# Performance work log

Measured on AMD Instinct MI355X. Metric: run time of the kernel, lower is better.

## Reference

```python
import jax, jax.numpy as jnp
import numpy as np

B, D_IN, D_H, N = 16, 32, 64, 4000
ORDER = 2
C_CAT = D_IN + D_H            # 96 channels into each gate conv
C_EFF = (ORDER + 1) * C_CAT   # 288 after order-K diffusion concat


def setup_inputs() -> dict:
    key = jax.random.key(0)
    ks = jax.random.split(key, 9)
    x = jax.random.normal(ks[0], (B, D_IN, N), dtype=jnp.float32)
    h = jax.random.normal(ks[1], (B, D_H, N), dtype=jnp.float32)
    # uniform adjacency, roughly row-normalized to keep diffusion stable
    adj = jax.random.uniform(ks[2], (N, N), dtype=jnp.float32) / N
    scale = 0.05
    Wf = jax.random.normal(ks[3], (D_H, C_EFF), dtype=jnp.float32) * scale
    Wu = jax.random.normal(ks[4], (D_H, C_EFF), dtype=jnp.float32) * scale
    Wc = jax.random.normal(ks[5], (D_H, C_EFF), dtype=jnp.float32) * scale
    bf = jax.random.normal(ks[6], (D_H,), dtype=jnp.float32) * scale
    bu = jax.random.normal(ks[7], (D_H,), dtype=jnp.float32) * scale
    bc = jax.random.normal(ks[8], (D_H,), dtype=jnp.float32) * scale
    return {"x": x, "h": h, "adj": adj, "Wf": Wf, "bf": bf,
            "Wu": Wu, "bu": bu, "Wc": Wc, "bc": bc}


def _spatial_conv(z, adj, W, b):
    # z: [b, c, n]; order-2 diffusion: concat [z, A z, A^2 z] then 1x1 conv
    z1 = jnp.einsum('mn,bcn->bcm', adj, z)
    z2 = jnp.einsum('mn,bcn->bcm', adj, z1)
    feats = jnp.concatenate([z, z1, z2], axis=1)           # [b, 3c, n]
    return jnp.einsum('oc,bcn->bon', W, feats) + b[None, :, None]


def reference(x, h, adj, Wf, bf, Wu, bu, Wc, bc):
    x_gates = jnp.concatenate([x, h], axis=1)              # [b, d_in+d_h, n]
    r = jax.nn.sigmoid(_spatial_conv(x_gates, adj, Wf, bf))
    u = jax.nn.sigmoid(_spatial_conv(x_gates, adj, Wu, bu))
    x_c = jnp.concatenate([x, r * h], axis=1)
    c = jnp.tanh(_spatial_conv(x_c, adj, Wc, bc))
    return u * h + (1.0 - u) * c
```

## Files before the change

kernel.cpp:

```cpp
#include <hip/hip_runtime.h>
#include <cstdint>


#define NREAL 4000
#define NPAD  4096

typedef unsigned short u16;
typedef __attribute__((ext_vector_type(8))) short short8;
typedef __attribute__((ext_vector_type(4))) float f32x4;
typedef __attribute__((ext_vector_type(4))) unsigned short u16x4;

__device__ __forceinline__ u16 f2bf(float f) {
  unsigned u = __builtin_bit_cast(unsigned, f);
  return (u16)((u + 0x7FFFu + ((u >> 16) & 1u)) >> 16);
}
__device__ __forceinline__ float bf2f(u16 b) {
  unsigned u = ((unsigned)b) << 16;
  return __builtin_bit_cast(float, u);
}

__global__ __launch_bounds__(256) void k_pack_adj(const float* __restrict__ adj,
                                                  u16* __restrict__ out) {
  const int idx = blockIdx.x * 256 + threadIdx.x;
  const int m = idx >> 10;
  const int n0 = (idx & 1023) << 2;
  u16x4 o;
  if (m < NREAL && n0 < NREAL) {
    const float4 v = *reinterpret_cast<const float4*>(&adj[(long)m * NREAL + n0]);
    o.x = f2bf(v.x); o.y = f2bf(v.y); o.z = f2bf(v.z); o.w = f2bf(v.w);
  } else {
    o.x = 0; o.y = 0; o.z = 0; o.w = 0;
  }
  *reinterpret_cast<u16x4*>(&out[(long)m * NPAD + n0]) = o;
}

__global__ __launch_bounds__(256) void k_pack_zg(const float* __restrict__ x,
                                                 const float* __restrict__ h,
                                                 u16* __restrict__ zg) {
  const int idx = blockIdx.x * 256 + threadIdx.x;
  const int row = idx >> 10;
  const int n0 = (idx & 1023) << 2;
  const int b = row / 96, c = row % 96;
  const float* src = (c < 32) ? &x[((long)b * 32 + c) * NREAL]
                              : &h[((long)b * 64 + (c - 32)) * NREAL];
  u16x4 o;
  if (n0 < NREAL) {
    const float4 v = *reinterpret_cast<const float4*>(&src[n0]);
    o.x = f2bf(v.x); o.y = f2bf(v.y); o.z = f2bf(v.z); o.w = f2bf(v.w);
  } else {
    o.x = 0; o.y = 0; o.z = 0; o.w = 0;
  }
  *reinterpret_cast<u16x4*>(&zg[(long)row * NPAD + n0]) = o;
}

__global__ __launch_bounds__(256) void k_pack_w(const float* __restrict__ Wf,
                                                const float* __restrict__ Wu,
                                                const float* __restrict__ Wc,
                                                float* __restrict__ Wgt,
                                                float* __restrict__ Wct) {
  const int idx = blockIdx.x * 256 + threadIdx.x;
  if (idx < 288 * 128) {
    const int c = idx >> 7, o = idx & 127;
    Wgt[idx] = (o < 64) ? Wf[o * 288 + c] : Wu[(o - 64) * 288 + c];
  }
  if (idx < 288 * 64) {
    const int c = idx >> 6, o = idx & 63;
    Wct[idx] = Wc[o * 288 + c];
  }
}

#define GLDS(dst, src)                                                         \
  __builtin_amdgcn_global_load_lds(                                            \
      (const __attribute__((address_space(1))) void*)(src),                    \
      (__attribute__((address_space(3))) void*)(dst), 16, 0, 0)

template<bool F32OUT>
__global__ __launch_bounds__(512, 2) void k_gemm256(const u16* __restrict__ A,
                                                    const u16* __restrict__ B,
                                                    void* __restrict__ Cout,
                                                    int ktPerChunk, long chunkElems) {
  __shared__ __align__(16) u16 As[2][256 * 64];
  __shared__ __align__(16) u16 Bs[2][256 * 64];
  const int tid = threadIdx.x;
  const int lane = tid & 63;
  const int wv = tid >> 6;
  const int wm = wv >> 2;
  const int wn = wv & 3;

  const int srow = tid >> 3;
  const int jlog = (tid & 7) ^ (srow & 7);
  const long kt0 = (long)blockIdx.z * ktPerChunk * 64;
  const u16* aB = A + (long)(blockIdx.y * 256 + srow) * NPAD + kt0 + jlog * 8;
  const u16* bB = B + (long)(blockIdx.x * 256 + srow) * NPAD + kt0 + jlog * 8;
  const int ldst = tid * 8;

  const int fr = lane & 15;
  const int swz = (fr & 7) << 4;
  const int kb0 = (((lane >> 4) << 4)) ^ swz;
  const int kb1 = (64 + ((lane >> 4) << 4)) ^ swz;

  f32x4 acc[8][4] = {};
  const int T = ktPerChunk;

  GLDS(&Bs[0][0 + ldst],     bB);
  GLDS(&Bs[0][4096 + ldst],  bB + 64L * NPAD);
  GLDS(&Bs[0][8192 + ldst],  bB + 128L * NPAD);
  GLDS(&Bs[0][12288 + ldst], bB + 192L * NPAD);
  GLDS(&As[0][0 + ldst],     aB);
  GLDS(&As[0][8192 + ldst],  aB + 128L * NPAD);
  GLDS(&As[0][4096 + ldst],  aB + 64L * NPAD);
  GLDS(&As[0][12288 + ldst], aB + 192L * NPAD);
  asm volatile("s_waitcnt vmcnt(0)" ::: "memory");
  __builtin_amdgcn_s_barrier();
  __builtin_amdgcn_sched_barrier(0);

  for (int t = 0; t < T; ++t) {
    const int bsel = t & 1;
    const char* Ab = (const char*)&As[bsel][0];
    const char* Bb = (const char*)&Bs[bsel][0];
    u16* An = &As[bsel ^ 1][0];
    u16* Bn = &Bs[bsel ^ 1][0];
    const bool more = (t + 1 < T);
    const long ko = (long)(t + 1) * 64;
    short8 bv[4][2];
#pragma unroll
    for (int p = 0; p < 4; ++p) {
      if (more) {
        if (p == 0) { GLDS(Bn + ldst, bB + ko);
                      GLDS(Bn + 4096 + ldst, bB + 64L * NPAD + ko); }
        if (p == 1) { GLDS(Bn + 8192 + ldst, bB + 128L * NPAD + ko);
                      GLDS(Bn + 12288 + ldst, bB + 192L * NPAD + ko); }
        if (p == 2) { GLDS(An + ldst, aB + ko);
                      GLDS(An + 8192 + ldst, aB + 128L * NPAD + ko); }
        if (p == 3) { GLDS(An + 4096 + ldst, aB + 64L * NPAD + ko);
                      GLDS(An + 12288 + ldst, aB + 192L * NPAD + ko); }
      }
      asm volatile("" ::: "memory");
      if (p == 0) {
#pragma unroll
        for (int ni = 0; ni < 4; ++ni) {
          const int brow = (wn << 6) + (ni << 4) + fr;
          bv[ni][0] = *(const short8*)(Bb + brow * 128 + kb0);
          bv[ni][1] = *(const short8*)(Bb + brow * 128 + kb1);
        }
      }
      short8 av[2][2];
#pragma unroll
      for (int q = 0; q < 2; ++q) {
        const int arow = (wm << 7) + ((2 * p + q) << 4) + fr;
        av[q][0] = *(const short8*)(Ab + arow * 128 + kb0);
        av[q][1] = *(const short8*)(Ab + arow * 128 + kb1);
      }
      __builtin_amdgcn_s_setprio(1);
#pragma unroll
      for (int q = 0; q < 2; ++q)
#pragma unroll
        for (int ni = 0; ni < 4; ++ni) {
          acc[2 * p + q][ni] = __builtin_amdgcn_mfma_f32_16x16x32_bf16(
              av[q][0], bv[ni][0], acc[2 * p + q][ni], 0, 0, 0);
          acc[2 * p + q][ni] = __builtin_amdgcn_mfma_f32_16x16x32_bf16(
              av[q][1], bv[ni][1], acc[2 * p + q][ni], 0, 0, 0);
        }
      __builtin_amdgcn_s_setprio(0);
      if (p == 1) {
        if (more) asm volatile("s_waitcnt vmcnt(4)" ::: "memory");
        else      asm volatile("s_waitcnt vmcnt(0)" ::: "memory");
        __builtin_amdgcn_s_barrier();
        __builtin_amdgcn_sched_barrier(0);
      }
      if (p == 3 && more) {
        asm volatile("s_waitcnt vmcnt(2)" ::: "memory");
        __builtin_amdgcn_s_barrier();
        __builtin_amdgcn_sched_barrier(0);
      }
    }
  }

  const int rb = blockIdx.y * 256 + (wm << 7) + ((lane >> 4) << 2);
  const int cb = blockIdx.x * 256 + (wn << 6) + fr;
  if (F32OUT) {
    float* C = (float*)Cout + (long)blockIdx.z * chunkElems;
#pragma unroll
    for (int mi = 0; mi < 8; ++mi)
#pragma unroll
      for (int ni = 0; ni < 4; ++ni)
#pragma unroll
        for (int q = 0; q < 4; ++q)
          C[(long)(rb + (mi << 4) + q) * NPAD + cb + (ni << 4)] = acc[mi][ni][q];
  } else {
    u16* C = (u16*)Cout;
#pragma unroll
    for (int mi = 0; mi < 8; ++mi)
#pragma unroll
      for (int ni = 0; ni < 4; ++ni)
#pragma unroll
        for (int q = 0; q < 4; ++q)
          C[(long)(rb + (mi << 4) + q) * NPAD + cb + (ni << 4)] = f2bf(acc[mi][ni][q]);
  }
}

template<int NC>
__global__ __launch_bounds__(256) void k_combine(const float* __restrict__ P,
                                                 long chunkElems,
                                                 u16* __restrict__ out) {
  const long i4 = ((long)blockIdx.x * 256 + threadIdx.x) * 4;
  f32x4 s = *reinterpret_cast<const f32x4*>(&P[i4]);
#pragma unroll
  for (int c = 1; c < NC; ++c) {
    const f32x4 v = *reinterpret_cast<const f32x4*>(&P[(long)c * chunkElems + i4]);
    s.x += v.x; s.y += v.y; s.z += v.z; s.w += v.w;
  }
  u16x4 o;
  o.x = f2bf(s.x); o.y = f2bf(s.y); o.z = f2bf(s.z); o.w = f2bf(s.w);
  *reinterpret_cast<u16x4*>(&out[i4]) = o;
}

__global__ __launch_bounds__(512) void k_gates(
    const float* __restrict__ x, const float* __restrict__ h,
    const float* __restrict__ Wgt,
    const float* __restrict__ bfv, const float* __restrict__ buv,
    const u16* __restrict__ Z1, const u16* __restrict__ Z2,
    u16* __restrict__ rh_bf, float* __restrict__ rh_f, float* __restrict__ u_f) {
  const int lane = threadIdx.x & 63;
  const int wq = __builtin_amdgcn_readfirstlane(threadIdx.x >> 6);
  const int b = blockIdx.y;
  const int n0 = blockIdx.x * 128 + (lane << 1);
  if (n0 >= NREAL) return;
  const int ob = wq << 4;
  const float* xb = x + (long)b * 32 * NREAL + n0;
  const float* hb = h + (long)b * 64 * NREAL + n0;
  const u16* z1b = Z1 + (long)b * 96 * NPAD + n0;
  const u16* z2b = Z2 + (long)b * 96 * NPAD + n0;

  float a0[16] = {}, a1[16] = {};
#pragma unroll 4
  for (int c = 0; c < 32; ++c) {
    const float2 f = *reinterpret_cast<const float2*>(&xb[(long)c * NREAL]);
#pragma unroll
    for (int oi = 0; oi < 16; ++oi) {
      const float w = Wgt[c * 128 + ob + oi];
      a0[oi] = fmaf(w, f.x, a0[oi]); a1[oi] = fmaf(w, f.y, a1[oi]);
    }
  }
#pragma unroll 4
  for (int c = 0; c < 64; ++c) {
    const float2 f = *reinterpret_cast<const float2*>(&hb[(long)c * NREAL]);
#pragma unroll
    for (int oi = 0; oi < 16; ++oi) {
      const float w = Wgt[(32 + c) * 128 + ob + oi];
      a0[oi] = fmaf(w, f.x, a0[oi]); a1[oi] = fmaf(w, f.y, a1[oi]);
    }
  }
#pragma unroll 4
  for (int c = 0; c < 96; ++c) {
    const unsigned pv = *reinterpret_cast<const unsigned*>(&z1b[(long)c * NPAD]);
    const float f0 = bf2f((u16)(pv & 0xffff)), f1 = bf2f((u16)(pv >> 16));
#pragma unroll
    for (int oi = 0; oi < 16; ++oi) {
      const float w = Wgt[(96 + c) * 128 + ob + oi];
      a0[oi] = fmaf(w, f0, a0[oi]); a1[oi] = fmaf(w, f1, a1[oi]);
    }
  }
#pragma unroll 4
  for (int c = 0; c < 96; ++c) {
    const unsigned pv = *reinterpret_cast<const unsigned*>(&z2b[(long)c * NPAD]);
    const float f0 = bf2f((u16)(pv & 0xffff)), f1 = bf2f((u16)(pv >> 16));
#pragma unroll
    for (int oi = 0; oi < 16; ++oi) {
      const float w = Wgt[(192 + c) * 128 + ob + oi];
      a0[oi] = fmaf(w, f0, a0[oi]); a1[oi] = fmaf(w, f1, a1[oi]);
    }
  }

  if (wq < 4) {
#pragma unroll
    for (int oi = 0; oi < 16; ++oi) {
      const int og = ob + oi;
      const float bb = bfv[og];
      const float r0 = 1.f / (1.f + __expf(-(a0[oi] + bb)));
      const float r1 = 1.f / (1.f + __expf(-(a1[oi] + bb)));
      const float2 hv = *reinterpret_cast<const float2*>(&hb[(long)og * NREAL]);
      const float rh0 = r0 * hv.x, rh1 = r1 * hv.y;
      if (rh_f)
        *reinterpret_cast<float2*>(&rh_f[((long)b * 64 + og) * NREAL + n0]) =
            make_float2(rh0, rh1);
      const unsigned pk = (unsigned)f2bf(rh0) | ((unsigned)f2bf(rh1) << 16);
      *reinterpret_cast<unsigned*>(&rh_bf[((long)b * 64 + og) * NPAD + n0]) = pk;
    }
  } else {
#pragma unroll
    for (int oi = 0; oi < 16; ++oi) {
      const int og = (ob - 64) + oi;
      const float bb = buv[og];
      const float u0 = 1.f / (1.f + __expf(-(a0[oi] + bb)));
      const float u1 = 1.f / (1.f + __expf(-(a1[oi] + bb)));
      *reinterpret_cast<float2*>(&u_f[((long)b * 64 + og) * NREAL + n0]) =
          make_float2(u0, u1);
    }
  }
}

template<bool RHF32>
__global__ __launch_bounds__(512) void k_cand(
    const float* __restrict__ x, const float* __restrict__ h,
    const float* __restrict__ Wct, const float* __restrict__ bcv,
    const u16* __restrict__ Z1, const u16* __restrict__ Z2,
    const u16* __restrict__ Rhb, const u16* __restrict__ Rh1,
    const u16* __restrict__ Rh2,
    const float* __restrict__ rh_f, const float* __restrict__ u_f,
    float* __restrict__ out) {
  const int lane = threadIdx.x & 63;
  const int wq = __builtin_amdgcn_readfirstlane(threadIdx.x >> 6);
  const int ob = (wq & 3) << 4;
  const int n = blockIdx.x * 128 + ((wq >> 2) << 6) + lane;
  const int b = blockIdx.y;
  if (n >= NREAL) return;
  const float* xb = x + (long)b * 32 * NREAL + n;
  const float* hb = h + (long)b * 64 * NREAL + n;
  const u16* z1b = Z1 + (long)b * 96 * NPAD + n;
  const u16* z2b = Z2 + (long)b * 96 * NPAD + n;
  const u16* r1b = Rh1 + (long)b * 64 * NPAD + n;
  const u16* r2b = Rh2 + (long)b * 64 * NPAD + n;
  const float* rfb = rh_f + (long)b * 64 * NREAL + n;
  const u16* rbb = Rhb + (long)b * 64 * NPAD + n;

  float acc[16] = {};
#pragma unroll 4
  for (int c = 0; c < 32; ++c) {
    const float f = xb[(long)c * NREAL];
#pragma unroll
    for (int oi = 0; oi < 16; ++oi)
      acc[oi] = fmaf(Wct[c * 64 + ob + oi], f, acc[oi]);
  }
#pragma unroll 4
  for (int c = 0; c < 64; ++c) {
    const float f = RHF32 ? rfb[(long)c * NREAL] : bf2f(rbb[(long)c * NPAD]);
#pragma unroll
    for (int oi = 0; oi < 16; ++oi)
      acc[oi] = fmaf(Wct[(32 + c) * 64 + ob + oi], f, acc[oi]);
  }
#pragma unroll 4
  for (int c = 0; c < 32; ++c) {
    const float f = bf2f(z1b[(long)c * NPAD]);
#pragma unroll
    for (int oi = 0; oi < 16; ++oi)
      acc[oi] = fmaf(Wct[(96 + c) * 64 + ob + oi], f, acc[oi]);
  }
#pragma unroll 4
  for (int c = 0; c < 64; ++c) {
    const float f = bf2f(r1b[(long)c * NPAD]);
#pragma unroll
    for (int oi = 0; oi < 16; ++oi)
      acc[oi] = fmaf(Wct[(128 + c) * 64 + ob + oi], f, acc[oi]);
  }
#pragma unroll 4
  for (int c = 0; c < 32; ++c) {
    const float f = bf2f(z2b[(long)c * NPAD]);
#pragma unroll
    for (int oi = 0; oi < 16; ++oi)
      acc[oi] = fmaf(Wct[(192 + c) * 64 + ob + oi], f, acc[oi]);
  }
#pragma unroll 4
  for (int c = 0; c < 64; ++c) {
    const float f = bf2f(r2b[(long)c * NPAD]);
#pragma unroll
    for (int oi = 0; oi < 16; ++oi)
      acc[oi] = fmaf(Wct[(224 + c) * 64 + ob + oi], f, acc[oi]);
  }

#pragma unroll
  for (int oi = 0; oi < 16; ++oi) {
    const int og = ob + oi;
    float v = acc[oi] + bcv[og];
    v = fminf(fmaxf(v, -15.f), 15.f);
    const float e2 = __expf(2.f * v);
    const float cv = (e2 - 1.f) / (e2 + 1.f);
    const float u = u_f[((long)b * 64 + og) * NREAL + n];
    out[((long)b * 64 + og) * NREAL + n] = u * hb[(long)og * NREAL] + (1.f - u) * cv;
  }
}

extern "C" void kernel_launch(void* const* d_in, const int* in_sizes, int n_in,
                              void* d_out, int out_size, void* d_ws, size_t ws_size,
                              hipStream_t stream) {
  const float* x   = (const float*)d_in[0];
  const float* h   = (const float*)d_in[1];
  const float* adj = (const float*)d_in[2];
  const float* Wf  = (const float*)d_in[3];
  const float* bf_ = (const float*)d_in[4];
  const float* Wu  = (const float*)d_in[5];
  const float* bu_ = (const float*)d_in[6];
  const float* Wc  = (const float*)d_in[7];
  const float* bc_ = (const float*)d_in[8];
  float* out = (float*)d_out;

  char* p = (char*)d_ws;
  auto alloc = [&](size_t bytes) { char* r = p; p += bytes; return r; };
  u16* adjb = (u16*)alloc((size_t)NPAD * NPAD * 2);
  u16* Zg   = (u16*)alloc((size_t)1536 * NPAD * 2);
  u16* Rhb  = Zg;
  u16* Z1   = (u16*)alloc((size_t)1536 * NPAD * 2);
  u16* Z2   = (u16*)alloc((size_t)1536 * NPAD * 2);
  u16* Rh1  = (u16*)alloc((size_t)1024 * NPAD * 2);
  u16* Rh2  = (u16*)alloc((size_t)1024 * NPAD * 2);
  float* uf = (float*)alloc((size_t)16 * 64 * NREAL * 4);
  float* Wgt = (float*)alloc(288 * 128 * 4);
  float* Wct = (float*)alloc(288 * 64 * 4);
  const size_t RHFB = (size_t)16 * 64 * NREAL * 4;
  size_t used = (size_t)(p - (char*)d_ws);
  float* rhf = nullptr;
  if (ws_size >= used + RHFB) rhf = (float*)alloc(RHFB);
  used = (size_t)(p - (char*)d_ws);

  const size_t PZ2 = (size_t)2 * 1536 * NPAD * 4;
  const size_t PR4 = (size_t)4 * 1024 * NPAD * 4;
  int sZ = 1, sR = 1;
  float* P = nullptr;
  if (ws_size >= used + PR4)      { P = (float*)alloc(PR4); sZ = 2; sR = 4; }
  else if (ws_size >= used + PZ2) { P = (float*)alloc(PZ2); sZ = 2; sR = 2; }

  auto gemm = [&](const u16* Ax, const u16* Bx, u16* Cb, int M, int sk) {
    const long ce = (long)M * NPAD;
    const int mt = M / 256;
    const int kpc = 64 / sk;
    if (sk == 4) {
      k_gemm256<true><<<dim3(16, mt, 4), 512, 0, stream>>>(Ax, Bx, P, kpc, ce);
      k_combine<4><<<dim3(M * 4), 256, 0, stream>>>(P, ce, Cb);
    } else if (sk == 2) {
      k_gemm256<true><<<dim3(16, mt, 2), 512, 0, stream>>>(Ax, Bx, P, kpc, ce);
      k_combine<2><<<dim3(M * 4), 256, 0, stream>>>(P, ce, Cb);
    } else {
      k_gemm256<false><<<dim3(16, mt, 1), 512, 0, stream>>>(Ax, Bx, Cb, 64, ce);
    }
  };

  k_pack_adj<<<dim3(NPAD * (NPAD / 4) / 256), 256, 0, stream>>>(adj, adjb);
  k_pack_zg <<<dim3(1536 * (NPAD / 4) / 256), 256, 0, stream>>>(x, h, Zg);
  k_pack_w  <<<dim3(144), 256, 0, stream>>>(Wf, Wu, Wc, Wgt, Wct);
  gemm(Zg, adjb, Z1, 1536, sZ);
  gemm(Z1, adjb, Z2, 1536, sZ);
  k_gates<<<dim3(32, 16), 512, 0, stream>>>(x, h, Wgt, bf_, bu_, Z1, Z2,
                                            Rhb, rhf, uf);
  gemm(Rhb, adjb, Rh1, 1024, sR);
  gemm(Rh1, adjb, Rh2, 1024, sR);
  if (rhf)
    k_cand<true><<<dim3(32, 16), 512, 0, stream>>>(x, h, Wct, bc_, Z1, Z2, Rhb,
                                                   Rh1, Rh2, rhf, uf, out);
  else
    k_cand<false><<<dim3(32, 16), 512, 0, stream>>>(x, h, Wct, bc_, Z1, Z2, Rhb,
                                                    Rh1, Rh2, rhf, uf, out);
}
```

Before: 544.6 us.

## Split GEMM into 8-phase barrier kernel for Z and simpler staged kernel for Rh

Adds a new GEMM kernel, k_gemm8p, that interleaves LDS reads, global-to-LDS prefetch and a barrier in each of four phases with explicit lgkmcnt waits. It is used for the two Z diffusion GEMMs. The existing k_gemm256 is rewritten into a simpler loop: it stages a whole k-tile into the other buffer, waits once, then runs two k-substeps of MFMA, and it handles the Rh GEMMs. The aim is better overlap of memory and MFMA work for each GEMM shape. The cost is more barriers in one kernel and coarser prefetch overlap in the other, and k_gemm8p drops the launch-bounds occupancy hint.

Result: faster. 482.5 us (-11.4%).

```diff
diff --git a/kernel.cpp b/kernel.cpp
--- a/kernel.cpp
+++ b/kernel.cpp
@@ -75,6 +75,129 @@
       (__attribute__((address_space(3))) void*)(dst), 16, 0, 0)
 
 template<bool F32OUT>
+__global__ __launch_bounds__(512) void k_gemm8p(const u16* __restrict__ A,
+                                                const u16* __restrict__ B,
+                                                void* __restrict__ Cout,
+                                                int ktPerChunk, long chunkElems) {
+  __shared__ __align__(16) u16 As[2][256 * 64];
+  __shared__ __align__(16) u16 Bs[2][256 * 64];
+  const int tid = threadIdx.x;
+  const int lane = tid & 63;
+  const int wv = tid >> 6;
+  const int wm = wv >> 2;
+  const int wn = wv & 3;
+
+  const int srow = tid >> 3;
+  const int jlog = (tid & 7) ^ (srow & 7);
+  const long kt0 = (long)blockIdx.z * ktPerChunk * 64;
+  const u16* aB = A + (long)(blockIdx.y * 256 + srow) * NPAD + kt0 + jlog * 8;
+  const u16* bB = B + (long)(blockIdx.x * 256 + srow) * NPAD + kt0 + jlog * 8;
+  const int ldst = tid * 8;
+
+  const int fr = lane & 15;
+  const int swz = (fr & 7) << 4;
+  const int kb0 = (((lane >> 4) << 4)) ^ swz;
+  const int kb1 = (64 + ((lane >> 4) << 4)) ^ swz;
+
+  f32x4 acc[8][4] = {};
+  const int T = ktPerChunk;
+
+  GLDS(&Bs[0][0 + ldst],     bB);
+  GLDS(&Bs[0][4096 + ldst],  bB + 64L * NPAD);
+  GLDS(&Bs[0][8192 + ldst],  bB + 128L * NPAD);
+  GLDS(&Bs[0][12288 + ldst], bB + 192L * NPAD);
+  GLDS(&As[0][0 + ldst],     aB);
+  GLDS(&As[0][8192 + ldst],  aB + 128L * NPAD);
+  GLDS(&As[0][4096 + ldst],  aB + 64L * NPAD);
+  GLDS(&As[0][12288 + ldst], aB + 192L * NPAD);
+  asm volatile("s_waitcnt vmcnt(0)" ::: "memory");
+  __builtin_amdgcn_s_barrier();
+
+  for (int t = 0; t < T; ++t) {
+    const int bs = t & 1;
+    const char* Ab = (const char*)&As[bs][0];
+    const char* Bb = (const char*)&Bs[bs][0];
+    u16* An = &As[bs ^ 1][0];
+    u16* Bn = &Bs[bs ^ 1][0];
+    const bool more = (t + 1 < T);
+    const long ko = (long)(t + 1) * 64;
+    short8 bv[4][2];
+#pragma unroll
+    for (int p = 0; p < 4; ++p) {
+      if (p == 0) {
+#pragma unroll
+        for (int ni = 0; ni < 4; ++ni) {
+          const int brow = (wn << 6) + (ni << 4) + fr;
+          bv[ni][0] = *(const short8*)(Bb + brow * 128 + kb0);
+          bv[ni][1] = *(const short8*)(Bb + brow * 128 + kb1);
+        }
+      }
+      short8 av[2][2];
+#pragma unroll
+      for (int q = 0; q < 2; ++q) {
+        const int arow = (wm << 7) + ((2 * p + q) << 4) + fr;
+        av[q][0] = *(const short8*)(Ab + arow * 128 + kb0);
+        av[q][1] = *(const short8*)(Ab + arow * 128 + kb1);
+      }
+      if (more) {
+        if (p == 0) { GLDS(Bn + ldst, bB + ko);
+                      GLDS(Bn + 4096 + ldst, bB + 64L * NPAD + ko); }
+        if (p == 1) { GLDS(Bn + 8192 + ldst, bB + 128L * NPAD + ko);
+                      GLDS(Bn + 12288 + ldst, bB + 192L * NPAD + ko); }
+        if (p == 2) { GLDS(An + ldst, aB + ko);
+                      GLDS(An + 8192 + ldst, aB + 128L * NPAD + ko); }
+        if (p == 3) { GLDS(An + 4096 + ldst, aB + 64L * NPAD + ko);
+                      GLDS(An + 12288 + ldst, aB + 192L * NPAD + ko); }
+      }
+      if (p == 0) asm volatile("s_waitcnt lgkmcnt(8)" ::: "memory");
+      __builtin_amdgcn_s_barrier();
+      asm volatile("s_waitcnt lgkmcnt(0)" ::: "memory");
+      __builtin_amdgcn_sched_barrier(0);
+      __builtin_amdgcn_s_setprio(1);
+#pragma unroll
+      for (int q = 0; q < 2; ++q)
+#pragma unroll
+        for (int ni = 0; ni < 4; ++ni) {
+          acc[2 * p + q][ni] = __builtin_amdgcn_mfma_f32_16x16x32_bf16(
+              av[q][0], bv[ni][0], acc[2 * p + q][ni], 0, 0, 0);
+          acc[2 * p + q][ni] = __builtin_amdgcn_mfma_f32_16x16x32_bf16(
+              av[q][1], bv[ni][1], acc[2 * p + q][ni], 0, 0, 0);
+        }
+      __builtin_amdgcn_s_setprio(0);
+      if (p == 1) {
+        if (more) asm volatile("s_waitcnt vmcnt(4)" ::: "memory");
+        else      asm volatile("s_waitcnt vmcnt(0)" ::: "memory");
+      }
+      if (p == 3 && more)
+        asm volatile("s_waitcnt vmcnt(2)" ::: "memory");
+      __builtin_amdgcn_s_barrier();
+    }
+  }
+
+  const int rb = blockIdx.y * 256 + (wm << 7) + ((lane >> 4) << 2);
+  const int cb = blockIdx.x * 256 + (wn << 6) + fr;
+  if (F32OUT) {
+    float* C = (float*)Cout + (long)blockIdx.z * chunkElems;
+#pragma unroll
+    for (int mi = 0; mi < 8; ++mi)
+#pragma unroll
+      for (int ni = 0; ni < 4; ++ni)
+#pragma unroll
+        for (int q = 0; q < 4; ++q)
+          C[(long)(rb + (mi << 4) + q) * NPAD + cb + (ni << 4)] = acc[mi][ni][q];
+  } else {
+    u16* C = (u16*)Cout;
+#pragma unroll
+    for (int mi = 0; mi < 8; ++mi)
+#pragma unroll
+      for (int ni = 0; ni < 4; ++ni)
+#pragma unroll
+        for (int q = 0; q < 4; ++q)
+          C[(long)(rb + (mi << 4) + q) * NPAD + cb + (ni << 4)] = f2bf(acc[mi][ni][q]);
+  }
+}
+
+template<bool F32OUT>
 __global__ __launch_bounds__(512, 2) void k_gemm256(const u16* __restrict__ A,
                                                     const u16* __restrict__ B,
                                                     void* __restrict__ Cout,
@@ -86,12 +209,13 @@
   const int wv = tid >> 6;
   const int wm = wv >> 2;
   const int wn = wv & 3;
+  const int bm = blockIdx.y, bn = blockIdx.x;
 
   const int srow = tid >> 3;
   const int jlog = (tid & 7) ^ (srow & 7);
   const long kt0 = (long)blockIdx.z * ktPerChunk * 64;
-  const u16* aB = A + (long)(blockIdx.y * 256 + srow) * NPAD + kt0 + jlog * 8;
-  const u16* bB = B + (long)(blockIdx.x * 256 + srow) * NPAD + kt0 + jlog * 8;
+  const u16* aS = A + (long)(bm * 256 + srow) * NPAD + kt0 + jlog * 8;
+  const u16* bS = B + (long)(bn * 256 + srow) * NPAD + kt0 + jlog * 8;
   const int ldst = tid * 8;
 
   const int fr = lane & 15;
@@ -100,84 +224,61 @@
   const int kb1 = (64 + ((lane >> 4) << 4)) ^ swz;
 
   f32x4 acc[8][4] = {};
-  const int T = ktPerChunk;
-
-  GLDS(&Bs[0][0 + ldst],     bB);
-  GLDS(&Bs[0][4096 + ldst],  bB + 64L * NPAD);
-  GLDS(&Bs[0][8192 + ldst],  bB + 128L * NPAD);
-  GLDS(&Bs[0][12288 + ldst], bB + 192L * NPAD);
-  GLDS(&As[0][0 + ldst],     aB);
-  GLDS(&As[0][8192 + ldst],  aB + 128L * NPAD);
-  GLDS(&As[0][4096 + ldst],  aB + 64L * NPAD);
-  GLDS(&As[0][12288 + ldst], aB + 192L * NPAD);
-  asm volatile("s_waitcnt vmcnt(0)" ::: "memory");
-  __builtin_amdgcn_s_barrier();
-  __builtin_amdgcn_sched_barrier(0);
-
-  for (int t = 0; t < T; ++t) {
-    const int bsel = t & 1;
-    const char* Ab = (const char*)&As[bsel][0];
-    const char* Bb = (const char*)&Bs[bsel][0];
-    u16* An = &As[bsel ^ 1][0];
-    u16* Bn = &Bs[bsel ^ 1][0];
-    const bool more = (t + 1 < T);
-    const long ko = (long)(t + 1) * 64;
-    short8 bv[4][2];
-#pragma unroll
-    for (int p = 0; p < 4; ++p) {
-      if (more) {
-        if (p == 0) { GLDS(Bn + ldst, bB + ko);
-                      GLDS(Bn + 4096 + ldst, bB + 64L * NPAD + ko); }
-        if (p == 1) { GLDS(Bn + 8192 + ldst, bB + 128L * NPAD + ko);
-                      GLDS(Bn + 12288 + ldst, bB + 192L * NPAD + ko); }
-        if (p == 2) { GLDS(An + ldst, aB + ko);
-                      GLDS(An + 8192 + ldst, aB + 128L * NPAD + ko); }
-        if (p == 3) { GLDS(An + 4096 + ldst, aB + 64L * NPAD + ko);
-                      GLDS(An + 12288 + ldst, aB + 192L * NPAD + ko); }
+
+#define STAGE2(buf, kk)                                                        \
+  {                                                                            \
+    const long ko2 = (long)(kk) * 64;                                          \
+    _Pragma("unroll")                                                          \
+    for (int i = 0; i < 4; ++i)                                                \
+      GLDS(&As[buf][i * 4096 + ldst], aS + (long)i * 64 * NPAD + ko2);         \
+    _Pragma("unroll")                                                          \
+    for (int i = 0; i < 4; ++i)                                                \
+      GLDS(&Bs[buf][i * 4096 + ldst], bS + (long)i * 64 * NPAD + ko2);         \
+  }
+
+  STAGE2(0, 0)
+  int cur = 0;
+  for (int kk = 0; kk < ktPerChunk; ++kk) {
+    if (kk + 1 < ktPerChunk) {
+      STAGE2(cur ^ 1, kk + 1)
+      asm volatile("s_waitcnt vmcnt(8)\ns_barrier" ::: "memory");
+    } else {
+      asm volatile("s_waitcnt vmcnt(0)\ns_barrier" ::: "memory");
+    }
+    const char* Ab = (const char*)&As[cur][0];
+    const char* Bb = (const char*)&Bs[cur][0];
+#pragma unroll
+    for (int ks = 0; ks < 2; ++ks) {
+      const int k2 = (ks == 0) ? 0 : 64;
+      short8 av[8], bv[4];
+#pragma unroll
+      for (int mi = 0; mi < 8; ++mi) {
+        const int row = (wm << 7) + (mi << 4) + fr;
+        av[mi] = *(const short8*)(Ab + row * 128 +
+                                  ((k2 + ((lane >> 4) << 4)) ^ ((row & 7) << 4)));
       }
-      asm volatile("" ::: "memory");
-      if (p == 0) {
-#pragma unroll
-        for (int ni = 0; ni < 4; ++ni) {
-          const int brow = (wn << 6) + (ni << 4) + fr;
-          bv[ni][0] = *(const short8*)(Bb + brow * 128 + kb0);
-          bv[ni][1] = *(const short8*)(Bb + brow * 128 + kb1);
-        }
-      }
-      short8 av[2][2];
-#pragma unroll
-      for (int q = 0; q < 2; ++q) {
-        const int arow = (wm << 7) + ((2 * p + q) << 4) + fr;
-        av[q][0] = *(const short8*)(Ab + arow * 128 + kb0);
-        av[q][1] = *(const short8*)(Ab + arow * 128 + kb1);
+#pragma unroll
+      for (int ni = 0; ni < 4; ++ni) {
+        const int row = (wn << 6) + (ni << 4) + fr;
+        bv[ni] = *(const short8*)(Bb + row * 128 +
+                                  ((k2 + ((lane >> 4) << 4)) ^ ((row & 7) << 4)));
       }
       __builtin_amdgcn_s_setprio(1);
 #pragma unroll
-      for (int q = 0; q < 2; ++q)
-#pragma unroll
-        for (int ni = 0; ni < 4; ++ni) {
-          acc[2 * p + q][ni] = __builtin_amdgcn_mfma_f32_16x16x32_bf16(
-              av[q][0], bv[ni][0], acc[2 * p + q][ni], 0, 0, 0);
-          acc[2 * p + q][ni] = __builtin_amdgcn_mfma_f32_16x16x32_bf16(
-              av[q][1], bv[ni][1], acc[2 * p + q][ni], 0, 0, 0);
-        }
+      for (int mi = 0; mi < 8; ++mi)
+#pragma unroll
+        for (int ni = 0; ni < 4; ++ni)
+          acc[mi][ni] = __builtin_amdgcn_mfma_f32_16x16x32_bf16(av[mi], bv[ni],
+                                                                acc[mi][ni], 0, 0, 0);
       __builtin_amdgcn_s_setprio(0);
-      if (p == 1) {
-        if (more) asm volatile("s_waitcnt vmcnt(4)" ::: "memory");
-        else      asm volatile("s_waitcnt vmcnt(0)" ::: "memory");
-        __builtin_amdgcn_s_barrier();
-        __builtin_amdgcn_sched_barrier(0);
-      }
-      if (p == 3 && more) {
-        asm volatile("s_waitcnt vmcnt(2)" ::: "memory");
-        __builtin_amdgcn_s_barrier();
-        __builtin_amdgcn_sched_barrier(0);
-      }
-    }
-  }
-
-  const int rb = blockIdx.y * 256 + (wm << 7) + ((lane >> 4) << 2);
-  const int cb = blockIdx.x * 256 + (wn << 6) + fr;
+    }
+    asm volatile("s_barrier" ::: "memory");
+    cur ^= 1;
+  }
+#undef STAGE2
+
+  const int rb = bm * 256 + (wm << 7) + ((lane >> 4) << 2);
+  const int cb = bn * 256 + (wn << 6) + fr;
   if (F32OUT) {
     float* C = (float*)Cout + (long)blockIdx.z * chunkElems;
 #pragma unroll
@@ -419,30 +520,37 @@
   if (ws_size >= used + PR4)      { P = (float*)alloc(PR4); sZ = 2; sR = 4; }
   else if (ws_size >= used + PZ2) { P = (float*)alloc(PZ2); sZ = 2; sR = 2; }
 
-  auto gemm = [&](const u16* Ax, const u16* Bx, u16* Cb, int M, int sk) {
-    const long ce = (long)M * NPAD;
-    const int mt = M / 256;
-    const int kpc = 64 / sk;
-    if (sk == 4) {
-      k_gemm256<true><<<dim3(16, mt, 4), 512, 0, stream>>>(Ax, Bx, P, kpc, ce);
-      k_combine<4><<<dim3(M * 4), 256, 0, stream>>>(P, ce, Cb);
-    } else if (sk == 2) {
-      k_gemm256<true><<<dim3(16, mt, 2), 512, 0, stream>>>(Ax, Bx, P, kpc, ce);
-      k_combine<2><<<dim3(M * 4), 256, 0, stream>>>(P, ce, Cb);
+  auto gemmZ = [&](const u16* Ax, const u16* Bx, u16* Cb) {
+    const long ce = (long)1536 * NPAD;
+    if (sZ == 2) {
+      k_gemm8p<true><<<dim3(16, 6, 2), 512, 0, stream>>>(Ax, Bx, P, 32, ce);
+      k_combine<2><<<dim3(1536 * 4), 256, 0, stream>>>(P, ce, Cb);
     } else {
-      k_gemm256<false><<<dim3(16, mt, 1), 512, 0, stream>>>(Ax, Bx, Cb, 64, ce);
+      k_gemm8p<false><<<dim3(16, 6, 1), 512, 0, stream>>>(Ax, Bx, Cb, 64, ce);
+    }
+  };
+  auto gemmR = [&](const u16* Ax, const u16* Bx, u16* Cb) {
+    const long ce = (long)1024 * NPAD;
+    if (sR == 4) {
+      k_gemm256<true><<<dim3(16, 4, 4), 512, 0, stream>>>(Ax, Bx, P, 16, ce);
+      k_combine<4><<<dim3(1024 * 4), 256, 0, stream>>>(P, ce, Cb);
+    } else if (sR == 2) {
+      k_gemm256<true><<<dim3(16, 4, 2), 512, 0, stream>>>(Ax, Bx, P, 32, ce);
+      k_combine<2><<<dim3(1024 * 4), 256, 0, stream>>>(P, ce, Cb);
+    } else {
+      k_gemm256<false><<<dim3(16, 4, 1), 512, 0, stream>>>(Ax, Bx, Cb, 64, ce);
     }
   };
 
   k_pack_adj<<<dim3(NPAD * (NPAD / 4) / 256), 256, 0, stream>>>(adj, adjb);
   k_pack_zg <<<dim3(1536 * (NPAD / 4) / 256), 256, 0, stream>>>(x, h, Zg);
   k_pack_w  <<<dim3(144), 256, 0, stream>>>(Wf, Wu, Wc, Wgt, Wct);
-  gemm(Zg, adjb, Z1, 1536, sZ);
-  gemm(Z1, adjb, Z2, 1536, sZ);
+  gemmZ(Zg, adjb, Z1);
+  gemmZ(Z1, adjb, Z2);
   k_gates<<<dim3(32, 16), 512, 0, stream>>>(x, h, Wgt, bf_, bu_, Z1, Z2,
                                             Rhb, rhf, uf);
-  gemm(Rhb, adjb, Rh1, 1024, sR);
-  gemm(Rh1, adjb, Rh2, 1024, sR);
+  gemmR(Rhb, adjb, Rh1);
+  gemmR(Rh1, adjb, Rh2);
   if (rhf)
     k_cand<true><<<dim3(32, 16), 512, 0, stream>>>(x, h, Wct, bc_, Z1, Z2, Rhb,
                                                    Rh1, Rh2, rhf, uf, out);
```

## Store split-K partials in bf16 and restructure GEMM LDS/barrier pipeline

Applied to the files above, without the earlier changes.

Split-K partial sums are now written as bf16 instead of fp32, which halves the partial write and read traffic, and the combine kernel reads 8-wide bf16 vectors. The Z GEMMs now use split-K 4 when workspace allows, instead of 2. The GEMM main loop now issues its LDS fragment reads before the async global-to-LDS prefetch and puts a barrier in every phase with explicit lgkmcnt waits. The occupancy hint of 2 blocks per SM is dropped. Rounding each partial to bf16 before summing loses some accuracy.

Measured after the change: 472.5 us. 1.15x faster.

```diff
diff --git a/kernel.cpp b/kernel.cpp
--- a/kernel.cpp
+++ b/kernel.cpp
@@ -9,6 +9,7 @@
 typedef __attribute__((ext_vector_type(8))) short short8;
 typedef __attribute__((ext_vector_type(4))) float f32x4;
 typedef __attribute__((ext_vector_type(4))) unsigned short u16x4;
+typedef __attribute__((ext_vector_type(8))) unsigned short u16x8;
 
 __device__ __forceinline__ u16 f2bf(float f) {
   unsigned u = __builtin_bit_cast(unsigned, f);
@@ -74,11 +75,10 @@
       (const __attribute__((address_space(1))) void*)(src),                    \
       (__attribute__((address_space(3))) void*)(dst), 16, 0, 0)
 
-template<bool F32OUT>
-__global__ __launch_bounds__(512, 2) void k_gemm256(const u16* __restrict__ A,
-                                                    const u16* __restrict__ B,
-                                                    void* __restrict__ Cout,
-                                                    int ktPerChunk, long chunkElems) {
+__global__ __launch_bounds__(512) void k_gemm8p(const u16* __restrict__ A,
+                                                const u16* __restrict__ B,
+                                                u16* __restrict__ Cout,
+                                                int ktPerChunk, long chunkElems) {
   __shared__ __align__(16) u16 As[2][256 * 64];
   __shared__ __align__(16) u16 Bs[2][256 * 64];
   const int tid = threadIdx.x;
@@ -112,19 +112,33 @@
   GLDS(&As[0][12288 + ldst], aB + 192L * NPAD);
   asm volatile("s_waitcnt vmcnt(0)" ::: "memory");
   __builtin_amdgcn_s_barrier();
-  __builtin_amdgcn_sched_barrier(0);
 
   for (int t = 0; t < T; ++t) {
-    const int bsel = t & 1;
-    const char* Ab = (const char*)&As[bsel][0];
-    const char* Bb = (const char*)&Bs[bsel][0];
-    u16* An = &As[bsel ^ 1][0];
-    u16* Bn = &Bs[bsel ^ 1][0];
+    const int bs = t & 1;
+    const char* Ab = (const char*)&As[bs][0];
+    const char* Bb = (const char*)&Bs[bs][0];
+    u16* An = &As[bs ^ 1][0];
+    u16* Bn = &Bs[bs ^ 1][0];
     const bool more = (t + 1 < T);
     const long ko = (long)(t + 1) * 64;
     short8 bv[4][2];
 #pragma unroll
     for (int p = 0; p < 4; ++p) {
+      if (p == 0) {
+#pragma unroll
+        for (int ni = 0; ni < 4; ++ni) {
+          const int brow = (wn << 6) + (ni << 4) + fr;
+          bv[ni][0] = *(const short8*)(Bb + brow * 128 + kb0);
+          bv[ni][1] = *(const short8*)(Bb + brow * 128 + kb1);
+        }
+      }
+      short8 av[2][2];
+#pragma unroll
+      for (int q = 0; q < 2; ++q) {
+        const int arow = (wm << 7) + ((2 * p + q) << 4) + fr;
+        av[q][0] = *(const short8*)(Ab + arow * 128 + kb0);
+        av[q][1] = *(const short8*)(Ab + arow * 128 + kb1);
+      }
       if (more) {
         if (p == 0) { GLDS(Bn + ldst, bB + ko);
                       GLDS(Bn + 4096 + ldst, bB + 64L * NPAD + ko); }
@@ -135,22 +149,10 @@
         if (p == 3) { GLDS(An + 4096 + ldst, aB + 64L * NPAD + ko);
                       GLDS(An + 12288 + ldst, aB + 192L * NPAD + ko); }
       }
-      asm volatile("" ::: "memory");
-      if (p == 0) {
-#pragma unroll
-        for (int ni = 0; ni < 4; ++ni) {
-          const int brow = (wn << 6) + (ni << 4) + fr;
-          bv[ni][0] = *(const short8*)(Bb + brow * 128 + kb0);
-          bv[ni][1] = *(const short8*)(Bb + brow * 128 + kb1);
-        }
-      }
-      short8 av[2][2];
-#pragma unroll
-      for (int q = 0; q < 2; ++q) {
-        const int arow = (wm << 7) + ((2 * p + q) << 4) + fr;
-        av[q][0] = *(const short8*)(Ab + arow * 128 + kb0);
-        av[q][1] = *(const short8*)(Ab + arow * 128 + kb1);
-      }
+      if (p == 0) asm volatile("s_waitcnt lgkmcnt(8)" ::: "memory");
+      __builtin_amdgcn_s_barrier();
+      asm volatile("s_waitcnt lgkmcnt(0)" ::: "memory");
+      __builtin_amdgcn_sched_barrier(0);
       __builtin_amdgcn_s_setprio(1);
 #pragma unroll
       for (int q = 0; q < 2; ++q)
@@ -165,54 +167,46 @@
       if (p == 1) {
         if (more) asm volatile("s_waitcnt vmcnt(4)" ::: "memory");
         else      asm volatile("s_waitcnt vmcnt(0)" ::: "memory");
-        __builtin_amdgcn_s_barrier();
-        __builtin_amdgcn_sched_barrier(0);
       }
-      if (p == 3 && more) {
+      if (p == 3 && more)
         asm volatile("s_waitcnt vmcnt(2)" ::: "memory");
-        __builtin_amdgcn_s_barrier();
-        __builtin_amdgcn_sched_barrier(0);
-      }
-    }
-  }
-
+      __builtin_amdgcn_s_barrier();
+    }
+  }
+
+  u16* C = Cout + (long)blockIdx.z * chunkElems;
   const int rb = blockIdx.y * 256 + (wm << 7) + ((lane >> 4) << 2);
   const int cb = blockIdx.x * 256 + (wn << 6) + fr;
-  if (F32OUT) {
-    float* C = (float*)Cout + (long)blockIdx.z * chunkElems;
-#pragma unroll
-    for (int mi = 0; mi < 8; ++mi)
-#pragma unroll
-      for (int ni = 0; ni < 4; ++ni)
-#pragma unroll
-        for (int q = 0; q < 4; ++q)
-          C[(long)(rb + (mi << 4) + q) * NPAD + cb + (ni << 4)] = acc[mi][ni][q];
-  } else {
-    u16* C = (u16*)Cout;
-#pragma unroll
-    for (int mi = 0; mi < 8; ++mi)
-#pragma unroll
-      for (int ni = 0; ni < 4; ++ni)
-#pragma unroll
-        for (int q = 0; q < 4; ++q)
-          C[(long)(rb + (mi << 4) + q) * NPAD + cb + (ni << 4)] = f2bf(acc[mi][ni][q]);
-  }
+#pragma unroll
+  for (int mi = 0; mi < 8; ++mi)
+#pragma unroll
+    for (int ni = 0; ni < 4; ++ni)
+#pragma unroll
+      for (int q = 0; q < 4; ++q)
+        C[(long)(rb + (mi << 4) + q) * NPAD + cb + (ni << 4)] = f2bf(acc[mi][ni][q]);
 }
 
 template<int NC>
-__global__ __launch_bounds__(256) void k_combine(const float* __restrict__ P,
-                                                 long chunkElems,
-                                                 u16* __restrict__ out) {
-  const long i4 = ((long)blockIdx.x * 256 + threadIdx.x) * 4;
-  f32x4 s = *reinterpret_cast<const f32x4*>(&P[i4]);
+__global__ __launch_bounds__(256) void k_combine_bf(const u16* __restrict__ P,
+                                                    long chunkElems,
+                                                    u16* __restrict__ out) {
+  const long i8 = ((long)blockIdx.x * 256 + threadIdx.x) * 8;
+  float s[8];
+  {
+    const u16x8 v = *reinterpret_cast<const u16x8*>(&P[i8]);
+#pragma unroll
+    for (int j = 0; j < 8; ++j) s[j] = bf2f(v[j]);
+  }
 #pragma unroll
   for (int c = 1; c < NC; ++c) {
-    const f32x4 v = *reinterpret_cast<const f32x4*>(&P[(long)c * chunkElems + i4]);
-    s.x += v.x; s.y += v.y; s.z += v.z; s.w += v.w;
-  }
-  u16x4 o;
-  o.x = f2bf(s.x); o.y = f2bf(s.y); o.z = f2bf(s.z); o.w = f2bf(s.w);
-  *reinterpret_cast<u16x4*>(&out[i4]) = o;
+    const u16x8 v = *reinterpret_cast<const u16x8*>(&P[(long)c * chunkElems + i8]);
+#pragma unroll
+    for (int j = 0; j < 8; ++j) s[j] += bf2f(v[j]);
+  }
+  u16x8 o;
+#pragma unroll
+  for (int j = 0; j < 8; ++j) o[j] = f2bf(s[j]);
+  *reinterpret_cast<u16x8*>(&out[i8]) = o;
 }
 
 __global__ __launch_bounds__(512) void k_gates(
@@ -412,37 +406,36 @@
   if (ws_size >= used + RHFB) rhf = (float*)alloc(RHFB);
   used = (size_t)(p - (char*)d_ws);
 
-  const size_t PZ2 = (size_t)2 * 1536 * NPAD * 4;
-  const size_t PR4 = (size_t)4 * 1024 * NPAD * 4;
-  int sZ = 1, sR = 1;
-  float* P = nullptr;
-  if (ws_size >= used + PR4)      { P = (float*)alloc(PR4); sZ = 2; sR = 4; }
-  else if (ws_size >= used + PZ2) { P = (float*)alloc(PZ2); sZ = 2; sR = 2; }
-
-  auto gemm = [&](const u16* Ax, const u16* Bx, u16* Cb, int M, int sk) {
+  const size_t PB4 = (size_t)4 * 1536 * NPAD * 2;
+  const size_t PB2 = (size_t)2 * 1536 * NPAD * 2;
+  int sK = 1;
+  u16* Pb = nullptr;
+  if (ws_size >= used + PB4)      { sK = 4; Pb = (u16*)alloc(PB4); }
+  else if (ws_size >= used + PB2) { sK = 2; Pb = (u16*)alloc(PB2); }
+
+  auto gemm = [&](const u16* Ax, const u16* Bx, u16* Cb, int M) {
     const long ce = (long)M * NPAD;
     const int mt = M / 256;
-    const int kpc = 64 / sk;
-    if (sk == 4) {
-      k_gemm256<true><<<dim3(16, mt, 4), 512, 0, stream>>>(Ax, Bx, P, kpc, ce);
-      k_combine<4><<<dim3(M * 4), 256, 0, stream>>>(P, ce, Cb);
-    } else if (sk == 2) {
-      k_gemm256<true><<<dim3(16, mt, 2), 512, 0, stream>>>(Ax, Bx, P, kpc, ce);
-      k_combine<2><<<dim3(M * 4), 256, 0, stream>>>(P, ce, Cb);
+    if (sK == 4) {
+      k_gemm8p<<<dim3(16, mt, 4), 512, 0, stream>>>(Ax, Bx, Pb, 16, ce);
+      k_combine_bf<4><<<dim3((int)(ce / 2048)), 256, 0, stream>>>(Pb, ce, Cb);
+    } else if (sK == 2) {
+      k_gemm8p<<<dim3(16, mt, 2), 512, 0, stream>>>(Ax, Bx, Pb, 32, ce);
+      k_combine_bf<2><<<dim3((int)(ce / 2048)), 256, 0, stream>>>(Pb, ce, Cb);
     } else {
-      k_gemm256<false><<<dim3(16, mt, 1), 512, 0, stream>>>(Ax, Bx, Cb, 64, ce);
+      k_gemm8p<<<dim3(16, mt, 1), 512, 0, stream>>>(Ax, Bx, Cb, 64, ce);
     }
   };
 
   k_pack_adj<<<dim3(NPAD * (NPAD / 4) / 256), 256, 0, stream>>>(adj, adjb);
   k_pack_zg <<<dim3(1536 * (NPAD / 4) / 256), 256, 0, stream>>>(x, h, Zg);
   k_pack_w  <<<dim3(144), 256, 0, stream>>>(Wf, Wu, Wc, Wgt, Wct);
-  gemm(Zg, adjb, Z1, 1536, sZ);
-  gemm(Z1, adjb, Z2, 1536, sZ);
+  gemm(Zg, adjb, Z1, 1536);
+  gemm(Z1, adjb, Z2, 1536);
   k_gates<<<dim3(32, 16), 512, 0, stream>>>(x, h, Wgt, bf_, bu_, Z1, Z2,
                                             Rhb, rhf, uf);
-  gemm(Rhb, adjb, Rh1, 1024, sR);
-  gemm(Rh1, adjb, Rh2, 1024, sR);
+  gemm(Rhb, adjb, Rh1, 1024);
+  gemm(Rh1, adjb, Rh2, 1024);
   if (rhf)
     k_cand<true><<<dim3(32, 16), 512, 0, stream>>>(x, h, Wct, bc_, Z1, Z2, Rhb,
                                                    Rh1, Rh2, rhf, uf, out);
```
